# Performance work log

Hardware: AMD Instinct MI355X
Metric: run time of the kernel (lower is better)

Reference implementation:

```python
import jax, jax.numpy as jnp
import numpy as np
from jax import lax

N, H, BS = 256, 1024, 128
ALPHA, BETA, SIGMA = 60.0, 20.0, 5.0
EPS = 1e-8


def _mlp_w(key, n_in, n_out):
    return jax.random.normal(key, (n_out, n_in), dtype=jnp.float32) / np.sqrt(n_in)


def setup_inputs() -> dict:
    key = jax.random.key(0)
    ks = jax.random.split(key, 8)
    inp = {
        "t": jnp.zeros((), dtype=jnp.float32),
        "x": jax.random.normal(ks[0], (BS, N), dtype=jnp.float32),
        "Wf1": _mlp_w(ks[1], N, H), "bf1": jnp.zeros((H,), jnp.float32),
        "Wf2": _mlp_w(ks[2], H, N), "bf2": jnp.zeros((N,), jnp.float32),
        "Wg1": _mlp_w(ks[3], N, H), "bg1": jnp.zeros((H,), jnp.float32),
        "Wg2": _mlp_w(ks[4], H, N), "bg2": jnp.zeros((N,), jnp.float32),
        "Wk1": _mlp_w(ks[5], N, H), "bk1": jnp.zeros((H,), jnp.float32),
        "Wk2": _mlp_w(ks[6], H, N), "bk2": jnp.zeros((N,), jnp.float32),
    }
    return inp


def reference(t, x, Wf1, bf1, Wf2, bf2, Wg1, bg1, Wg2, bg2, Wk1, bk1, Wk2, bk2):
    def mlp(u, W1, b1, W2, b2):
        return jnp.tanh(u @ W1.T + b1) @ W2.T + b2

    def k_func(u):
        return mlp(u, Wk1, bk1, Wk2, bk2)

    f_out = mlp(x, Wf1, bf1, Wf2, bf2)          # f_model(t, x); t unused
    k_out = k_func(x)
    G_k_out = mlp(x, Wg1, bg1, Wg2, bg2)        # g_fn(x)[0]
    dx_dt = f_out + G_k_out

    # compute_k_jacobian: torch detaches u, so no grad flows to x here.
    # torch layout: J[b, j, i] = d k_i / d u_j  (transpose of jacfwd output)
    x_d = lax.stop_gradient(x)
    J_fwd = jax.vmap(jax.jacfwd(k_func))(x_d)   # [bs, i_out, j_in]
    J_x = jnp.swapaxes(J_fwd, 1, 2)             # [bs, j, i]

    k_norm = jnp.linalg.norm(k_out, axis=1)                      # [bs]
    Jf = jnp.einsum('bji,bi->bj', J_x, f_out)                    # bmm(J, f)
    Jf_norm = jnp.linalg.norm(Jf, axis=1)
    c1 = Jf_norm - ALPHA * k_norm ** (2 * SIGMA - 1)
    JG = jnp.einsum('bji,bi->bj', J_x, G_k_out)                  # bmm(J, G)
    c2 = jnp.sum(k_out * JG, axis=1) - BETA * k_norm ** (2 * SIGMA)

    mask = (c1 > EPS) | (c2 < -EPS)                              # [bs]
    dx_upd = jnp.where(mask[:, None], jnp.zeros_like(dx_dt), dx_dt)
    return (dx_upd + dx_dt) / 2
```

## Files before the change

kernel.cpp:

```cpp
#include <hip/hip_runtime.h>
#include <stdint.h>

#define N_ 256
#define H_ 1024
#define BS_ 128

#define WS_SK    0
#define WS_OACC  131072
#define WS_OPART 229376
#define WS_JPART 1802240
#define WS_FLOATS 2850816

__global__ __launch_bounds__(512) void k12_l1l2(
    const float* __restrict__ x,
    const float* __restrict__ Wf1, const float* __restrict__ bf1,
    const float* __restrict__ Wg1, const float* __restrict__ bg1,
    const float* __restrict__ Wk1, const float* __restrict__ bk1,
    const float* __restrict__ Wf2, const float* __restrict__ bf2,
    const float* __restrict__ Wg2, const float* __restrict__ bg2,
    const float* __restrict__ Wk2, const float* __restrict__ bk2,
    float* __restrict__ sk, float* __restrict__ opart)
{
    const int bx = blockIdx.x;
    const int g  = bx % 48;
    const int rt = bx / 48;
    const int m  = g >> 4;
    const int ht = g & 15;
    const int t  = threadIdx.x;
    const int h0 = ht * 64;
    const int r0 = rt * 16;

    const float* W1 = (m == 0) ? Wf1 : (m == 1) ? Wg1 : Wk1;
    const float* b1 = (m == 0) ? bf1 : (m == 1) ? bg1 : bk1;
    const float* W2 = (m == 0) ? Wf2 : (m == 1) ? Wg2 : Wk2;
    const float* b2 = (m == 0) ? bf2 : (m == 1) ? bg2 : bk2;

    __shared__ __align__(16) float xs[16][256];
    __shared__ __align__(16) float ts[16][64];
    for (int u = t; u < 1024; u += 512)
        ((float4*)xs)[u] = ((const float4*)(x + r0 * N_))[u];
    __syncthreads();

    {
        const int hl = t & 63;
        const int rq = (t >> 6) * 2;
        const int h  = h0 + hl;
        float a0 = b1[h], a1 = a0;
        const float4* w4 = (const float4*)(W1 + h * N_);
        const float4* x0 = (const float4*)xs[rq];
        const float4* x1 = (const float4*)xs[rq + 1];
        #pragma unroll 8
        for (int c = 0; c < 64; ++c) {
            float4 w = w4[c];
            float4 p = x0[c];
            a0 += w.x * p.x + w.y * p.y + w.z * p.z + w.w * p.w;
            float4 q = x1[c];
            a1 += w.x * q.x + w.y * q.y + w.z * q.z + w.w * q.w;
        }
        const float v0 = tanhf(a0), v1 = tanhf(a1);
        ts[rq][hl] = v0; ts[rq + 1][hl] = v1;
        if (m == 2) {
            sk[(r0 + rq) * H_ + h]     = 1.0f - v0 * v0;
            sk[(r0 + rq + 1) * H_ + h] = 1.0f - v1 * v1;
        }
    }
    __syncthreads();

    {
        const int i  = t & 255;
        const int hf = (t >> 8) * 8;
        float acc[8];
        const float bv = (ht == 0) ? b2[i] : 0.0f;
        #pragma unroll
        for (int r = 0; r < 8; ++r) acc[r] = bv;

        const float4* w4 = (const float4*)(W2 + i * H_ + h0);
        #pragma unroll 2
        for (int c = 0; c < 16; ++c) {
            float4 w = w4[c];
            #pragma unroll
            for (int r = 0; r < 8; ++r) {
                float4 a = ((const float4*)ts[hf + r])[c];
                acc[r] += w.x * a.x + w.y * a.y + w.z * a.z + w.w * a.w;
            }
        }
        #pragma unroll
        for (int r = 0; r < 8; ++r)
            opart[((ht * 3 + m) * BS_ + r0 + hf + r) * N_ + i] = acc[r];
    }
}

__global__ __launch_bounds__(256) void k25_reduce(
    const float* __restrict__ opart, float* __restrict__ oacc)
{
    const int tid = blockIdx.x * 256 + threadIdx.x;
    float s = 0.f;
    #pragma unroll
    for (int ks = 0; ks < 16; ++ks)
        s += opart[ks * (3 * BS_ * N_) + tid];
    oacc[tid] = s;
}

__global__ __launch_bounds__(256) void k3_vj(
    const float* __restrict__ Wk1, const float* __restrict__ Wk2,
    const float* __restrict__ oacc, const float* __restrict__ sk,
    float* __restrict__ jpart)
{
    const int q  = blockIdx.x & 15;
    const int rp = blockIdx.x >> 4;
    const int t  = threadIdx.x;
    const int r0 = rp * 4;
    const int h0 = q * 64;

    __shared__ float fos[4][256], gos[4][256];
    __shared__ float sfv[4][64], sgv[4][64];

    for (int u = t; u < 1024; u += 256) {
        const int r = u >> 8, i = u & 255;
        fos[r][i] = oacc[(r0 + r) * N_ + i];
        gos[r][i] = oacc[(BS_ + r0 + r) * N_ + i];
    }
    __syncthreads();

    {
        const int hl = t & 63;
        const int rl = t >> 6;
        const int h  = h0 + hl;
        const float* w2 = Wk2 + h;
        float vf = 0.f, vg = 0.f;
        #pragma unroll 8
        for (int c = 0; c < 64; ++c) {
            const float4 of = ((const float4*)fos[rl])[c];
            const float4 og = ((const float4*)gos[rl])[c];
            const float w0 = w2[(4 * c + 0) * H_];
            const float w1 = w2[(4 * c + 1) * H_];
            const float w2v = w2[(4 * c + 2) * H_];
            const float w3 = w2[(4 * c + 3) * H_];
            vf += of.x * w0 + of.y * w1 + of.z * w2v + of.w * w3;
            vg += og.x * w0 + og.y * w1 + og.z * w2v + og.w * w3;
        }
        const float s = sk[(r0 + rl) * H_ + h];
        sfv[rl][hl] = s * vf;
        sgv[rl][hl] = s * vg;
    }
    __syncthreads();

    {
        float jf[4] = {0.f, 0.f, 0.f, 0.f};
        float jg[4] = {0.f, 0.f, 0.f, 0.f};
        const float* w1 = Wk1 + h0 * N_ + t;
        #pragma unroll 4
        for (int c = 0; c < 16; ++c) {
            const float w0 = w1[(4 * c + 0) * N_];
            const float wv1 = w1[(4 * c + 1) * N_];
            const float wv2 = w1[(4 * c + 2) * N_];
            const float wv3 = w1[(4 * c + 3) * N_];
            #pragma unroll
            for (int r = 0; r < 4; ++r) {
                const float4 sf = ((const float4*)sfv[r])[c];
                const float4 sg = ((const float4*)sgv[r])[c];
                jf[r] += sf.x * w0 + sf.y * wv1 + sf.z * wv2 + sf.w * wv3;
                jg[r] += sg.x * w0 + sg.y * wv1 + sg.z * wv2 + sg.w * wv3;
            }
        }
        #pragma unroll
        for (int r = 0; r < 4; ++r) {
            jpart[((q * 2 + 0) * BS_ + r0 + r) * N_ + t] = jf[r];
            jpart[((q * 2 + 1) * BS_ + r0 + r) * N_ + t] = jg[r];
        }
    }
}

__global__ __launch_bounds__(256) void k4_final(
    const float* __restrict__ oacc,
    const float* __restrict__ jpart,
    float* __restrict__ out)
{
    const int r = blockIdx.x;
    const int t = threadIdx.x;
    __shared__ float red[12];

    const float fo = oacc[r * N_ + t];
    const float go = oacc[(BS_ + r) * N_ + t];
    const float ko = oacc[(2 * BS_ + r) * N_ + t];

    float jf = 0.f, jg = 0.f;
    #pragma unroll
    for (int q = 0; q < 16; ++q) {
        jf += jpart[((q * 2 + 0) * BS_ + r) * N_ + t];
        jg += jpart[((q * 2 + 1) * BS_ + r) * N_ + t];
    }

    float v0 = ko * ko, v1 = jf * jf, v2 = ko * jg;
    #pragma unroll
    for (int o = 32; o > 0; o >>= 1) {
        v0 += __shfl_xor(v0, o, 64);
        v1 += __shfl_xor(v1, o, 64);
        v2 += __shfl_xor(v2, o, 64);
    }
    const int wid = t >> 6;
    if ((t & 63) == 0) {
        red[wid * 3 + 0] = v0;
        red[wid * 3 + 1] = v1;
        red[wid * 3 + 2] = v2;
    }
    __syncthreads();
    const float kn2 = red[0] + red[3] + red[6] + red[9];
    const float jf2 = red[1] + red[4] + red[7] + red[10];
    const float kjg = red[2] + red[5] + red[8] + red[11];

    const float knorm = sqrtf(kn2);
    const float kn4 = kn2 * kn2;
    const float kn8 = kn4 * kn4;
    const float c1 = sqrtf(jf2) - 60.0f * kn8 * knorm;
    const float c2 = kjg - 20.0f * kn8 * kn2;
    const float scale = ((c1 > 1e-8f) || (c2 < -1e-8f)) ? 0.5f : 1.0f;

    out[r * N_ + t] = (fo + go) * scale;
}

__global__ __launch_bounds__(256) void manifold_fused(
    const float* __restrict__ x,
    const float* __restrict__ Wf1, const float* __restrict__ bf1v,
    const float* __restrict__ Wf2, const float* __restrict__ bf2v,
    const float* __restrict__ Wg1, const float* __restrict__ bg1v,
    const float* __restrict__ Wg2, const float* __restrict__ bg2v,
    const float* __restrict__ Wk1, const float* __restrict__ bk1v,
    const float* __restrict__ Wk2, const float* __restrict__ bk2v,
    float* __restrict__ out)
{
    const int b = blockIdx.x;
    const int t = threadIdx.x;
    __shared__ float xs[N_];
    __shared__ float tf[H_], tg[H_], tk[H_], sk[H_];
    __shared__ float fo[N_], go[N_];
    __shared__ float sfv[H_], sgv[H_];
    __shared__ float red[12];

    xs[t] = x[b * N_ + t];
    __syncthreads();
    {
        float acc[12];
        const float4* rows[12];
        #pragma unroll
        for (int m = 0; m < 4; ++m) {
            const int h = t + m * 256;
            rows[m]     = (const float4*)(Wf1 + h * N_);
            rows[4 + m] = (const float4*)(Wg1 + h * N_);
            rows[8 + m] = (const float4*)(Wk1 + h * N_);
            acc[m] = bf1v[h]; acc[4 + m] = bg1v[h]; acc[8 + m] = bk1v[h];
        }
        const float4* xs4 = (const float4*)xs;
        #pragma unroll 2
        for (int c = 0; c < 64; ++c) {
            float4 a = xs4[c];
            #pragma unroll
            for (int r = 0; r < 12; ++r) {
                float4 w = rows[r][c];
                acc[r] += w.x * a.x + w.y * a.y + w.z * a.z + w.w * a.w;
            }
        }
        #pragma unroll
        for (int m = 0; m < 4; ++m) {
            const int h = t + m * 256;
            float vtf = tanhf(acc[m]);
            float vtg = tanhf(acc[4 + m]);
            float vtk = tanhf(acc[8 + m]);
            tf[h] = vtf; tg[h] = vtg; tk[h] = vtk; sk[h] = 1.0f - vtk * vtk;
        }
    }
    __syncthreads();
    float af = bf2v[t], ag = bg2v[t], ak = bk2v[t];
    {
        const float4* rf = (const float4*)(Wf2 + t * H_);
        const float4* rg = (const float4*)(Wg2 + t * H_);
        const float4* rk = (const float4*)(Wk2 + t * H_);
        #pragma unroll 2
        for (int c = 0; c < 256; ++c) {
            float4 wf = rf[c], wg = rg[c], wk = rk[c];
            float4 vf = ((const float4*)tf)[c];
            af += wf.x*vf.x + wf.y*vf.y + wf.z*vf.z + wf.w*vf.w;
            float4 vg = ((const float4*)tg)[c];
            ag += wg.x*vg.x + wg.y*vg.y + wg.z*vg.z + wg.w*vg.w;
            float4 vk = ((const float4*)tk)[c];
            ak += wk.x*vk.x + wk.y*vk.y + wk.z*vk.z + wk.w*vk.w;
        }
    }
    fo[t] = af; go[t] = ag;
    __syncthreads();
    {
        float vf[4] = {0.f,0.f,0.f,0.f}, vg[4] = {0.f,0.f,0.f,0.f};
        const float* base = Wk2 + 4 * t;
        #pragma unroll 4
        for (int i = 0; i < N_; ++i) {
            float4 w = *(const float4*)(base + i * H_);
            float fv = fo[i], gv = go[i];
            vf[0]+=w.x*fv; vf[1]+=w.y*fv; vf[2]+=w.z*fv; vf[3]+=w.w*fv;
            vg[0]+=w.x*gv; vg[1]+=w.y*gv; vg[2]+=w.z*gv; vg[3]+=w.w*gv;
        }
        #pragma unroll
        for (int c = 0; c < 4; ++c) {
            sfv[4*t+c] = sk[4*t+c]*vf[c];
            sgv[4*t+c] = sk[4*t+c]*vg[c];
        }
    }
    __syncthreads();
    float jf = 0.f, jg = 0.f;
    {
        const float* col = Wk1 + t;
        #pragma unroll 4
        for (int c = 0; c < 256; ++c) {
            float4 s4 = ((const float4*)sfv)[c];
            float4 g4 = ((const float4*)sgv)[c];
            const int h = c * 4;
            float w0 = col[(h+0)*N_], w1 = col[(h+1)*N_];
            float w2 = col[(h+2)*N_], w3 = col[(h+3)*N_];
            jf += s4.x*w0 + s4.y*w1 + s4.z*w2 + s4.w*w3;
            jg += g4.x*w0 + g4.y*w1 + g4.z*w2 + g4.w*w3;
        }
    }
    float v0 = ak*ak, v1 = jf*jf, v2 = ak*jg;
    #pragma unroll
    for (int o = 32; o > 0; o >>= 1) {
        v0 += __shfl_xor(v0, o, 64);
        v1 += __shfl_xor(v1, o, 64);
        v2 += __shfl_xor(v2, o, 64);
    }
    const int wid = t >> 6;
    if ((t & 63) == 0) {
        red[wid*3+0] = v0; red[wid*3+1] = v1; red[wid*3+2] = v2;
    }
    __syncthreads();
    const float kn2 = red[0]+red[3]+red[6]+red[9];
    const float jf2 = red[1]+red[4]+red[7]+red[10];
    const float kjg = red[2]+red[5]+red[8]+red[11];
    const float knorm = sqrtf(kn2);
    const float kn4 = kn2*kn2, kn8 = kn4*kn4;
    const float c1 = sqrtf(jf2) - 60.0f*kn8*knorm;
    const float c2 = kjg - 20.0f*kn8*kn2;
    const float scale = ((c1 > 1e-8f) || (c2 < -1e-8f)) ? 0.5f : 1.0f;
    out[b*N_+t] = (af+ag)*scale;
}

extern "C" void kernel_launch(void* const* d_in, const int* in_sizes, int n_in,
                              void* d_out, int out_size, void* d_ws, size_t ws_size,
                              hipStream_t stream) {
    const float* x    = (const float*)d_in[1];
    const float* Wf1  = (const float*)d_in[2];
    const float* bf1v = (const float*)d_in[3];
    const float* Wf2  = (const float*)d_in[4];
    const float* bf2v = (const float*)d_in[5];
    const float* Wg1  = (const float*)d_in[6];
    const float* bg1v = (const float*)d_in[7];
    const float* Wg2  = (const float*)d_in[8];
    const float* bg2v = (const float*)d_in[9];
    const float* Wk1  = (const float*)d_in[10];
    const float* bk1v = (const float*)d_in[11];
    const float* Wk2  = (const float*)d_in[12];
    const float* bk2v = (const float*)d_in[13];
    float* out = (float*)d_out;

    if (ws_size < (size_t)WS_FLOATS * sizeof(float)) {
        manifold_fused<<<BS_, 256, 0, stream>>>(
            x, Wf1, bf1v, Wf2, bf2v, Wg1, bg1v, Wg2, bg2v,
            Wk1, bk1v, Wk2, bk2v, out);
        return;
    }

    float* ws    = (float*)d_ws;
    float* sk    = ws + WS_SK;
    float* oacc  = ws + WS_OACC;
    float* opart = ws + WS_OPART;
    float* jpart = ws + WS_JPART;

    k12_l1l2  <<<384, 512, 0, stream>>>(x, Wf1, bf1v, Wg1, bg1v, Wk1, bk1v,
                                        Wf2, bf2v, Wg2, bg2v, Wk2, bk2v,
                                        sk, opart);
    k25_reduce<<<384, 256, 0, stream>>>(opart, oacc);
    k3_vj     <<<512, 256, 0, stream>>>(Wk1, Wk2, oacc, sk, jpart);
    k4_final  <<<BS_, 256, 0, stream>>>(oacc, jpart, out);
}
```

Measured before the change: 139.7 us.

## Replace fp32 MLP layer kernel with split-bf16 MFMA matrix-core path

Adds a prep kernel that splits x and all layer weights into high and low bf16 halves, stored in MFMA-fragment-friendly tiled layouts. The fused layer1/layer2 kernel then uses 16x16x32 bf16 MFMA with three products (hi*hi, hi*lo, lo*hi) to approximate fp32 accuracy. The tanh activations are staged in swizzled LDS. The aim is to move the FP32 FMA work onto the matrix cores. In exchange it adds an extra launch that re-converts the weights on every call and extra workspace traffic, and it carries a small precision risk from dropping the lo*lo term.

```diff
diff --git a/kernel.cpp b/kernel.cpp
--- a/kernel.cpp
+++ b/kernel.cpp
@@ -9,84 +9,164 @@
 #define WS_OACC  131072
 #define WS_OPART 229376
 #define WS_JPART 1802240
-#define WS_FLOATS 2850816
-
-__global__ __launch_bounds__(512) void k12_l1l2(
+#define WS_XH    2850816
+#define WS_XL    2867200
+#define WS_W1H   2883584
+#define WS_W1L   3276800
+#define WS_W2H   3670016
+#define WS_W2L   4063232
+#define WS_FLOATS 4456448
+
+typedef __attribute__((ext_vector_type(8))) short short8v;
+typedef __attribute__((ext_vector_type(4))) float f32x4;
+
+__device__ __forceinline__ ushort bhi(float v) {
+    return (ushort)(__float_as_uint(v) >> 16);
+}
+__device__ __forceinline__ float btrunc(float v) {
+    return __uint_as_float(__float_as_uint(v) & 0xFFFF0000u);
+}
+
+__global__ __launch_bounds__(256) void kprep(
     const float* __restrict__ x,
-    const float* __restrict__ Wf1, const float* __restrict__ bf1,
-    const float* __restrict__ Wg1, const float* __restrict__ bg1,
-    const float* __restrict__ Wk1, const float* __restrict__ bk1,
-    const float* __restrict__ Wf2, const float* __restrict__ bf2,
-    const float* __restrict__ Wg2, const float* __restrict__ bg2,
-    const float* __restrict__ Wk2, const float* __restrict__ bk2,
+    const float* __restrict__ Wf1, const float* __restrict__ Wg1,
+    const float* __restrict__ Wk1,
+    const float* __restrict__ Wf2, const float* __restrict__ Wg2,
+    const float* __restrict__ Wk2,
+    ushort* __restrict__ xh, ushort* __restrict__ xl,
+    ushort* __restrict__ w1h, ushort* __restrict__ w1l,
+    ushort* __restrict__ w2h, ushort* __restrict__ w2l)
+{
+    const int T = blockIdx.x * 4 + (threadIdx.x >> 6);
+    const int l = threadIdx.x & 63;
+    const int c16 = l & 15, g = l >> 4;
+
+    const float* src;
+    ushort *ph, *pl;
+    int dst;
+    if (T < 64) {
+        const int rt = T >> 3, ks = T & 7;
+        src = x + (rt * 16 + c16) * N_ + ks * 32 + g * 8;
+        dst = (T * 64 + l) * 8;
+        ph = xh; pl = xl;
+    } else if (T < 64 + 1536) {
+        const int T2 = T - 64;
+        const int m = T2 >> 9, rem = T2 & 511;
+        const int htg = rem >> 3, ks = rem & 7;
+        const float* W1 = (m == 0) ? Wf1 : (m == 1) ? Wg1 : Wk1;
+        src = W1 + (htg * 16 + c16) * N_ + ks * 32 + g * 8;
+        dst = ((m << 15) + rem * 64 + l) * 8;
+        ph = w1h; pl = w1l;
+    } else {
+        const int T3 = T - 64 - 1536;
+        const int m = T3 >> 9, rem = T3 & 511;
+        const int it = rem >> 5, hk = rem & 31;
+        const float* W2 = (m == 0) ? Wf2 : (m == 1) ? Wg2 : Wk2;
+        src = W2 + (it * 16 + c16) * H_ + hk * 32 + g * 8;
+        dst = ((m << 15) + rem * 64 + l) * 8;
+        ph = w2h; pl = w2l;
+    }
+    const float4 a = *(const float4*)src;
+    const float4 b = *(const float4*)(src + 4);
+    const float s[8] = {a.x, a.y, a.z, a.w, b.x, b.y, b.z, b.w};
+    union { short8v v; ushort u[8]; } H, L;
+    #pragma unroll
+    for (int i = 0; i < 8; ++i) {
+        H.u[i] = bhi(s[i]);
+        L.u[i] = bhi(s[i] - btrunc(s[i]));
+    }
+    *(short8v*)(ph + dst) = H.v;
+    *(short8v*)(pl + dst) = L.v;
+}
+
+__global__ __launch_bounds__(256) void k12m(
+    const ushort* __restrict__ xh, const ushort* __restrict__ xl,
+    const ushort* __restrict__ w1h, const ushort* __restrict__ w1l,
+    const ushort* __restrict__ w2h, const ushort* __restrict__ w2l,
+    const float* __restrict__ bf1, const float* __restrict__ bg1,
+    const float* __restrict__ bk1,
+    const float* __restrict__ bf2, const float* __restrict__ bg2,
+    const float* __restrict__ bk2,
     float* __restrict__ sk, float* __restrict__ opart)
 {
-    const int bx = blockIdx.x;
-    const int g  = bx % 48;
-    const int rt = bx / 48;
-    const int m  = g >> 4;
-    const int ht = g & 15;
-    const int t  = threadIdx.x;
-    const int h0 = ht * 64;
+    const int bx  = blockIdx.x;
+    const int sid = (bx & 7) * 48 + (bx >> 3);
+    const int m   = sid >> 7;
+    const int rem = sid & 127;
+    const int hs  = rem >> 3;
+    const int rt  = rem & 7;
+    const int t = threadIdx.x, w = t >> 6, l = t & 63;
+    const int col = l & 15, g = l >> 4;
     const int r0 = rt * 16;
 
-    const float* W1 = (m == 0) ? Wf1 : (m == 1) ? Wg1 : Wk1;
     const float* b1 = (m == 0) ? bf1 : (m == 1) ? bg1 : bk1;
-    const float* W2 = (m == 0) ? Wf2 : (m == 1) ? Wg2 : Wk2;
     const float* b2 = (m == 0) ? bf2 : (m == 1) ? bg2 : bk2;
 
-    __shared__ __align__(16) float xs[16][256];
-    __shared__ __align__(16) float ts[16][64];
-    for (int u = t; u < 1024; u += 512)
-        ((float4*)xs)[u] = ((const float4*)(x + r0 * N_))[u];
-    __syncthreads();
-
-    {
-        const int hl = t & 63;
-        const int rq = (t >> 6) * 2;
-        const int h  = h0 + hl;
-        float a0 = b1[h], a1 = a0;
-        const float4* w4 = (const float4*)(W1 + h * N_);
-        const float4* x0 = (const float4*)xs[rq];
-        const float4* x1 = (const float4*)xs[rq + 1];
-        #pragma unroll 8
-        for (int c = 0; c < 64; ++c) {
-            float4 w = w4[c];
-            float4 p = x0[c];
-            a0 += w.x * p.x + w.y * p.y + w.z * p.z + w.w * p.w;
-            float4 q = x1[c];
-            a1 += w.x * q.x + w.y * q.y + w.z * q.z + w.w * q.w;
-        }
-        const float v0 = tanhf(a0), v1 = tanhf(a1);
-        ts[rq][hl] = v0; ts[rq + 1][hl] = v1;
-        if (m == 2) {
-            sk[(r0 + rq) * H_ + h]     = 1.0f - v0 * v0;
-            sk[(r0 + rq + 1) * H_ + h] = 1.0f - v1 * v1;
-        }
-    }
-    __syncthreads();
-
-    {
-        const int i  = t & 255;
-        const int hf = (t >> 8) * 8;
-        float acc[8];
-        const float bv = (ht == 0) ? b2[i] : 0.0f;
-        #pragma unroll
-        for (int r = 0; r < 8; ++r) acc[r] = bv;
-
-        const float4* w4 = (const float4*)(W2 + i * H_ + h0);
-        #pragma unroll 2
-        for (int c = 0; c < 16; ++c) {
-            float4 w = w4[c];
-            #pragma unroll
-            for (int r = 0; r < 8; ++r) {
-                float4 a = ((const float4*)ts[hf + r])[c];
-                acc[r] += w.x * a.x + w.y * a.y + w.z * a.z + w.w * a.w;
-            }
-        }
-        #pragma unroll
-        for (int r = 0; r < 8; ++r)
-            opart[((ht * 3 + m) * BS_ + r0 + hf + r) * N_ + i] = acc[r];
+    const short8v* XH  = (const short8v*)xh;
+    const short8v* XL  = (const short8v*)xl;
+    const short8v* W1H = (const short8v*)w1h + m * 32768;
+    const short8v* W1L = (const short8v*)w1l + m * 32768;
+    const short8v* W2H = (const short8v*)w2h + m * 32768;
+    const short8v* W2L = (const short8v*)w2l + m * 32768;
+
+    __shared__ __align__(16) ushort tsh[1024], tsl[1024];
+
+    const int htile = hs * 4 + w;
+    f32x4 acc1 = {0.f, 0.f, 0.f, 0.f};
+    #pragma unroll
+    for (int ks = 0; ks < 8; ++ks) {
+        const short8v axh = XH[(rt * 8 + ks) * 64 + l];
+        const short8v axl = XL[(rt * 8 + ks) * 64 + l];
+        const short8v bh  = W1H[(htile * 8 + ks) * 64 + l];
+        const short8v bl  = W1L[(htile * 8 + ks) * 64 + l];
+        acc1 = __builtin_amdgcn_mfma_f32_16x16x32_bf16(axl, bh, acc1, 0, 0, 0);
+        acc1 = __builtin_amdgcn_mfma_f32_16x16x32_bf16(axh, bl, acc1, 0, 0, 0);
+        acc1 = __builtin_amdgcn_mfma_f32_16x16x32_bf16(axh, bh, acc1, 0, 0, 0);
+    }
+    {
+        const int h  = htile * 16 + col;
+        const float bv = b1[h];
+        const int hl_ = w * 16 + col;
+        const int cb = hl_ >> 3, wi = hl_ & 7;
+        #pragma unroll
+        for (int j = 0; j < 4; ++j) {
+            const int row = g * 4 + j;
+            const float v = tanhf(acc1[j] + bv);
+            if (m == 2) sk[(r0 + row) * H_ + h] = 1.0f - v * v;
+            const int cs = cb ^ (row & 7);
+            tsh[row * 64 + cs * 8 + wi] = bhi(v);
+            tsl[row * 64 + cs * 8 + wi] = bhi(v - btrunc(v));
+        }
+    }
+    __syncthreads();
+
+    f32x4 acc2[4] = {{0.f,0.f,0.f,0.f}, {0.f,0.f,0.f,0.f},
+                     {0.f,0.f,0.f,0.f}, {0.f,0.f,0.f,0.f}};
+    #pragma unroll
+    for (int ks2 = 0; ks2 < 2; ++ks2) {
+        const int cs = (ks2 * 4 + g) ^ (col & 7);
+        const short8v ath = *(const short8v*)&tsh[col * 64 + cs * 8];
+        const short8v atl = *(const short8v*)&tsl[col * 64 + cs * 8];
+        const int hk = hs * 2 + ks2;
+        #pragma unroll
+        for (int n = 0; n < 4; ++n) {
+            const int itg = w * 4 + n;
+            const short8v bh = W2H[(itg * 32 + hk) * 64 + l];
+            const short8v bl = W2L[(itg * 32 + hk) * 64 + l];
+            acc2[n] = __builtin_amdgcn_mfma_f32_16x16x32_bf16(atl, bh, acc2[n], 0, 0, 0);
+            acc2[n] = __builtin_amdgcn_mfma_f32_16x16x32_bf16(ath, bl, acc2[n], 0, 0, 0);
+            acc2[n] = __builtin_amdgcn_mfma_f32_16x16x32_bf16(ath, bh, acc2[n], 0, 0, 0);
+        }
+    }
+    #pragma unroll
+    for (int n = 0; n < 4; ++n) {
+        const int i = (w * 4 + n) * 16 + col;
+        const float bias = (hs == 0) ? b2[i] : 0.0f;
+        #pragma unroll
+        for (int j = 0; j < 4; ++j) {
+            const int row = g * 4 + j;
+            opart[((hs * 3 + m) * BS_ + r0 + row) * N_ + i] = acc2[n][j] + bias;
+        }
     }
 }
 
@@ -132,12 +212,12 @@
         for (int c = 0; c < 64; ++c) {
             const float4 of = ((const float4*)fos[rl])[c];
             const float4 og = ((const float4*)gos[rl])[c];
-            const float w0 = w2[(4 * c + 0) * H_];
-            const float w1 = w2[(4 * c + 1) * H_];
+            const float w0  = w2[(4 * c + 0) * H_];
+            const float w1v = w2[(4 * c + 1) * H_];
             const float w2v = w2[(4 * c + 2) * H_];
-            const float w3 = w2[(4 * c + 3) * H_];
-            vf += of.x * w0 + of.y * w1 + of.z * w2v + of.w * w3;
-            vg += og.x * w0 + og.y * w1 + og.z * w2v + og.w * w3;
+            const float w3  = w2[(4 * c + 3) * H_];
+            vf += of.x * w0 + of.y * w1v + of.z * w2v + of.w * w3;
+            vg += og.x * w0 + og.y * w1v + og.z * w2v + og.w * w3;
         }
         const float s = sk[(r0 + rl) * H_ + h];
         sfv[rl][hl] = s * vf;
@@ -151,7 +231,7 @@
         const float* w1 = Wk1 + h0 * N_ + t;
         #pragma unroll 4
         for (int c = 0; c < 16; ++c) {
-            const float w0 = w1[(4 * c + 0) * N_];
+            const float w0  = w1[(4 * c + 0) * N_];
             const float wv1 = w1[(4 * c + 1) * N_];
             const float wv2 = w1[(4 * c + 2) * N_];
             const float wv3 = w1[(4 * c + 3) * N_];
@@ -372,9 +452,17 @@
     float* oacc  = ws + WS_OACC;
     float* opart = ws + WS_OPART;
     float* jpart = ws + WS_JPART;
-
-    k12_l1l2  <<<384, 512, 0, stream>>>(x, Wf1, bf1v, Wg1, bg1v, Wk1, bk1v,
-                                        Wf2, bf2v, Wg2, bg2v, Wk2, bk2v,
+    ushort* xh  = (ushort*)(ws + WS_XH);
+    ushort* xl  = (ushort*)(ws + WS_XL);
+    ushort* w1h = (ushort*)(ws + WS_W1H);
+    ushort* w1l = (ushort*)(ws + WS_W1L);
+    ushort* w2h = (ushort*)(ws + WS_W2H);
+    ushort* w2l = (ushort*)(ws + WS_W2L);
+
+    kprep     <<<784, 256, 0, stream>>>(x, Wf1, Wg1, Wk1, Wf2, Wg2, Wk2,
+                                        xh, xl, w1h, w1l, w2h, w2l);
+    k12m      <<<384, 256, 0, stream>>>(xh, xl, w1h, w1l, w2h, w2l,
+                                        bf1v, bg1v, bk1v, bf2v, bg2v, bk2v,
                                         sk, opart);
     k25_reduce<<<384, 256, 0, stream>>>(opart, oacc);
     k3_vj     <<<512, 256, 0, stream>>>(Wk1, Wk2, oacc, sk, jpart);
```

Result: faster. 114.8 us (-17.8%).
